# Performance work log

Hardware: AMD Instinct MI355X
Metric: run time of the kernel (lower is better)

## Reference

```python
import jax, jax.numpy as jnp
import numpy as np

B, LQ, LK, D = 8, 1024, 4096, 1024


def setup_inputs() -> dict:
    key = jax.random.key(0)
    k1, k2, k3, k4, k5, k6 = jax.random.split(key, 6)
    s = 1.0 / np.sqrt(D)
    return {
        "T": jax.random.normal(k1, (B, LQ, D), dtype=jnp.float32),
        "S": jax.random.normal(k2, (B, LK, D), dtype=jnp.float32),
        "Wq": jax.random.uniform(k3, (D, D), jnp.float32, -s, s),
        "Wk": jax.random.uniform(k4, (D, D), jnp.float32, -s, s),
        "Wv": jax.random.uniform(k5, (D, D), jnp.float32, -s, s),
        "Wo": jax.random.uniform(k6, (D, D), jnp.float32, -s, s),
    }


def reference(T, S, Wq, Wk, Wv, Wo):
    # Linear layers: y = x @ W.T (torch nn.Linear convention), bias=False
    q = jnp.einsum('bqd,ed->bqe', T, Wq)          # [B, LQ, D]
    k = jnp.einsum('bkd,ed->bke', S, Wk)          # [B, LK, D]
    v = jnp.einsum('bkd,ed->bke', S, Wv)          # [B, LK, D]
    scale = jnp.asarray(D, q.dtype) ** -0.5        # hidden_dim ** -0.5 (single head)
    attn = jnp.einsum('bqe,bke->bqk', q, k) * scale  # [B, LQ, LK]
    attn = jax.nn.softmax(attn, axis=-1)
    out = jnp.einsum('bqk,bke->bqe', attn, v)      # [B, LQ, D]
    return jnp.einsum('bqe,fe->bqf', out, Wo)      # output projection
```

## Files before the change

### kernel.cpp

```cpp
#include <hip/hip_runtime.h>
#include <stdint.h>

typedef __bf16 bf16;
typedef __bf16 bf16x8 __attribute__((ext_vector_type(8)));
typedef float f32x4 __attribute__((ext_vector_type(4)));

__device__ __forceinline__ void gload_lds16(const void* g, void* l) {
    __builtin_amdgcn_global_load_lds(
        (const __attribute__((address_space(1))) unsigned int*)g,
        (__attribute__((address_space(3))) unsigned int*)l, 16, 0, 0);
}

#define BAR()    asm volatile("s_barrier" ::: "memory")
#define WAITV(N) asm volatile("s_waitcnt vmcnt(" #N ")" ::: "memory")

#define STG(S, R, G, KOFF2, RS) do { \
    const bf16* _g = (G) + (KOFF2); \
    gload_lds16(_g,      &lds[S][R][d0]); \
    gload_lds16(_g + RS, &lds[S][R][d1]); \
  } while (0)

#define RD(S, R, OFF) (*(const bf16x8*)((const char*)&lds[S][R][0] + (OFF)))

#define MM(MB) \
    __builtin_amdgcn_s_setprio(1); \
    _Pragma("unroll") for (int mi = 0; mi < 4; ++mi) \
      _Pragma("unroll") for (int nj = 0; nj < 4; ++nj) \
        acc[MB + mi][nj] = __builtin_amdgcn_mfma_f32_16x16x32_bf16(av[mi], bv[nj], acc[MB + mi][nj], 0, 0, 0); \
    __builtin_amdgcn_s_setprio(0);

#define PH1(S, STGX) { \
    _Pragma("unroll") for (int nj = 0; nj < 4; ++nj) bv[nj] = RD(S, 2, bBase + nj * 1024); \
    _Pragma("unroll") for (int mi = 0; mi < 4; ++mi) av[mi] = RD(S, 0, aBase + mi * 1024); \
    STGX; BAR(); MM(0) BAR(); }

#define PH2(S, STGX) { \
    _Pragma("unroll") for (int mi = 0; mi < 4; ++mi) av[mi] = RD(S, 0, aBase + 4096 + mi * 1024); \
    STGX; BAR(); MM(4) BAR(); }

#define PH3(S, STGX) { \
    _Pragma("unroll") for (int nj = 0; nj < 4; ++nj) bv[nj] = RD(S, 3, bBase + nj * 1024); \
    _Pragma("unroll") for (int mi = 0; mi < 4; ++mi) av[mi] = RD(S, 1, aBase + mi * 1024); \
    STGX; BAR(); MM(0) BAR(); }

#define PH4(S, STGX, WT) { \
    _Pragma("unroll") for (int mi = 0; mi < 4; ++mi) av[mi] = RD(S, 1, aBase + 4096 + mi * 1024); \
    STGX; BAR(); MM(4) WT; BAR(); }

__global__ __launch_bounds__(512, 2)
void gemm_qkv(const bf16* __restrict__ Tb, const bf16* __restrict__ Sb,
              const bf16* __restrict__ Wq, const bf16* __restrict__ Wk,
              const bf16* __restrict__ Wv,
              bf16* __restrict__ Qo, bf16* __restrict__ Ko, bf16* __restrict__ VTo)
{
    __shared__ __align__(16) bf16 lds[2][4][8192];

    const int nwg  = gridDim.x;
    const int orig = blockIdx.x;
    const int q8   = nwg >> 3, r8 = nwg & 7;
    const int xcd  = orig & 7, lid = orig >> 3;
    const int p    = (xcd < r8 ? xcd * (q8 + 1) : r8 * (q8 + 1) + (xcd - r8) * q8) + lid;

    const bf16 *A, *Bw; bf16 *Co; bool vt = false;
    int lp;
    if (p < 512)       { lp = p;        A = Sb; Bw = Wk; Co = Ko; }
    else if (p < 1024) { lp = p - 512;  A = Sb; Bw = Wv; Co = VTo; vt = true; }
    else               { lp = p - 1024; A = Tb; Bw = Wq; Co = Qo; }

    const long rowb = (long)(lp >> 2) << 8;
    const long colb = (long)(lp & 3) << 8;

    const int t  = threadIdx.x;
    const int l  = t & 63;
    const int w  = t >> 6;
    const int wm = w >> 2;
    const int wn = w & 3;
    const int l15 = l & 15;
    const int r0  = (l >> 4) << 2;

    const int sL   = (t * 16) ^ (((t >> 3) & 3) << 4);
    const int srow = sL >> 6;
    const int sk   = (sL & 63) >> 1;
    const bf16* gA = A + (rowb + srow) * 1024 + sk;
    const bf16* gB = Bw + (colb + srow) * 1024 + sk;
    const long rA = 131072, rB = 131072;
    const int  d0 = t * 8, d1 = t * 8 + 4096;

    const int xl    = ((l >> 1) & 3) << 4;
    const int aBase = ((wm * 128 + l15) * 64 + ((l >> 4) << 4)) ^ xl;
    const int bBase = ((wn * 64  + l15) * 64 + ((l >> 4) << 4)) ^ xl;

    f32x4 acc[8][4] = {};
    bf16x8 av[4], bv[4];

    STG(0, 0, gA, 0,  rA);
    STG(0, 1, gA, 32, rA);
    STG(0, 2, gB, 0,  rB);
    STG(0, 3, gB, 32, rB);
    STG(1, 2, gB, 64, rB);
    STG(1, 0, gA, 64, rA);
    STG(1, 3, gB, 96, rB);
    WAITV(6);
    BAR();

    for (int i = 0; i < 7; ++i) {
        const int kb = i << 7;
        const int kn = kb + 128;
        PH1(0, STG(1, 1, gA, kb + 96, rA));
        PH2(0, STG(0, 2, gB, kn,      rB));
        PH3(0, STG(0, 0, gA, kn,      rA));
        PH4(0, STG(0, 3, gB, kn + 32, rB), WAITV(6));
        PH1(1, STG(0, 1, gA, kn + 32, rA));
        PH2(1, STG(1, 2, gB, kn + 64, rB));
        PH3(1, STG(1, 0, gA, kn + 64, rA));
        PH4(1, STG(1, 3, gB, kn + 96, rB), WAITV(6));
    }
    {
        PH1(0, STG(1, 1, gA, 7 * 128 + 96, rA));
        PH2(0, );
        PH3(0, );
        PH4(0, , WAITV(0));
        PH1(1, );
        PH2(1, );
        PH3(1, );
        PH4(1, , );
    }

    bf16* epi = &lds[0][0][0];
    const int rrow   = t >> 5;
    const int cchunk = (t & 31) << 3;
    const int myh = vt ? (wn >> 1) : wm;
#pragma unroll
    for (int h = 0; h < 2; ++h) {
        if (myh == h) {
#pragma unroll
            for (int mf = 0; mf < 8; ++mf)
#pragma unroll
              for (int nj = 0; nj < 4; ++nj)
#pragma unroll
                for (int r = 0; r < 4; ++r) {
                    int orow = wm * 128 + mf * 16 + r0 + r;
                    int ocol = wn * 64 + nj * 16 + l15;
                    if (vt) { int tmp = orow; orow = ocol; ocol = tmp; }
                    epi[(orow - h * 128) * 280 + ocol] = (bf16)acc[mf][nj][r];
                }
        }
        __syncthreads();
#pragma unroll
        for (int pp = 0; pp < 8; ++pp) {
            const int lrow = pp * 16 + rrow;
            const int row  = h * 128 + lrow;
            uint4 d = *(const uint4*)&epi[lrow * 280 + cchunk];
            if (!vt) {
                *(uint4*)&Co[(rowb + row) * 1024 + colb + cchunk] = d;
            } else {
                const long zz  = rowb >> 12;
                const long lk0 = (rowb & 4095) + cchunk;
                *(uint4*)&Co[zz * 4194304L + (colb + row) * 4096L + lk0] = d;
            }
        }
        __syncthreads();
    }
}

template<int OMODE>
__global__ __launch_bounds__(512, 2)
void gemm256(const bf16* __restrict__ A, const bf16* __restrict__ B,
             void* __restrict__ Cv, int K, int N,
             long batchA, long batchB, long batchC, float alpha,
             int nbx, int nby, int GC, int lda, int ldb,
             float* __restrict__ Smp)
{
    __shared__ __align__(16) bf16 lds[2][4][8192];

    const int nwg  = gridDim.x;
    const int orig = blockIdx.x;
    const int q8   = nwg >> 3, r8 = nwg & 7;
    const int xcd  = orig & 7, lid = orig >> 3;
    int p = (xcd < r8 ? xcd * (q8 + 1) : r8 * (q8 + 1) + (xcd - r8) * q8) + lid;

    int hv = 0;
    if constexpr (OMODE == 3) { hv = p >> 7; p &= 127; }
    const int kOff = hv << 11;

    const int perb = nbx * nby;
    const int z    = p / perb;
    const int pb   = p - z * perb;
    const int sw   = nby * GC;
    const int st   = pb / sw;
    const int rem  = pb - st * sw;
    const int by   = rem / GC;
    const int bx   = st * GC + (rem - by * GC);

    const long rowb = (long)by << 8;
    const long colb = (long)bx << 8;

    const int t  = threadIdx.x;
    const int l  = t & 63;
    const int w  = t >> 6;
    const int wm = w >> 2;
    const int wn = w & 3;
    const int l15 = l & 15;
    const int r0  = (l >> 4) << 2;

    const int sL   = (t * 16) ^ (((t >> 3) & 3) << 4);
    const int srow = sL >> 6;
    const int sk   = (sL & 63) >> 1;
    const bf16* gA = A + (long)z * batchA + (rowb + srow) * (long)lda + sk + kOff;
    const bf16* gB = B + (long)z * batchB + (colb + srow) * (long)ldb + sk + kOff;
    const long rA = 128L * lda;
    const long rB = 128L * ldb;
    const int  d0 = t * 8, d1 = t * 8 + 4096;

    const int xl    = ((l >> 1) & 3) << 4;
    const int aBase = ((wm * 128 + l15) * 64 + ((l >> 4) << 4)) ^ xl;
    const int bBase = ((wn * 64  + l15) * 64 + ((l >> 4) << 4)) ^ xl;

    f32x4 acc[8][4] = {};
    bf16x8 av[4], bv[4];

    STG(0, 0, gA, 0,  rA);
    STG(0, 1, gA, 32, rA);
    STG(0, 2, gB, 0,  rB);
    STG(0, 3, gB, 32, rB);
    STG(1, 2, gB, 64, rB);
    STG(1, 0, gA, 64, rA);
    STG(1, 3, gB, 96, rB);
    WAITV(6);
    BAR();

    const int NI = K >> 7;
    for (int i = 0; i < NI - 1; ++i) {
        const int kb = i << 7;
        const int kn = kb + 128;
        PH1(0, STG(1, 1, gA, kb + 96, rA));
        PH2(0, STG(0, 2, gB, kn,      rB));
        PH3(0, STG(0, 0, gA, kn,      rA));
        PH4(0, STG(0, 3, gB, kn + 32, rB), WAITV(6));
        PH1(1, STG(0, 1, gA, kn + 32, rA));
        PH2(1, STG(1, 2, gB, kn + 64, rB));
        PH3(1, STG(1, 0, gA, kn + 64, rA));
        PH4(1, STG(1, 3, gB, kn + 96, rB), WAITV(6));
    }
    {
        const int kb = (NI - 1) << 7;
        PH1(0, STG(1, 1, gA, kb + 96, rA));
        PH2(0, );
        PH3(0, );
        PH4(0, , WAITV(0));
        PH1(1, );
        PH2(1, );
        PH3(1, );
        PH4(1, , );
    }

    if constexpr (OMODE == 2) {
        const long cb0 = colb + wn * 64 + l15;
        const long rb0 = rowb + wm * 128 + r0;
#pragma unroll
        for (int mf = 0; mf < 8; ++mf)
#pragma unroll
          for (int nj = 0; nj < 4; ++nj) {
            const long col = cb0 + nj * 16;
#pragma unroll
            for (int r = 0; r < 4; ++r)
                ((float*)Cv)[(long)z * batchC + (rb0 + mf * 16 + r) * (long)N + col]
                    = acc[mf][nj][r] * alpha;
          }
    } else {
        bf16* Cb;
        if constexpr (OMODE == 3)
            Cb = (bf16*)Cv + (long)hv * 8388608 + (long)z * 1048576;
        else
            Cb = (bf16*)Cv + (long)z * batchC;
        bf16* epi = &lds[0][0][0];
        const int rrow   = t >> 5;
        const int cchunk = (t & 31) << 3;
#pragma unroll
        for (int h = 0; h < 2; ++h) {
            if (wm == h) {
#pragma unroll
                for (int mf = 0; mf < 8; ++mf)
#pragma unroll
                  for (int nj = 0; nj < 4; ++nj)
#pragma unroll
                    for (int r = 0; r < 4; ++r) {
                        float v = acc[mf][nj][r];
                        if constexpr (OMODE == 4) v = __expf(v * alpha);
                        const int orow = wm * 128 + mf * 16 + r0 + r;
                        const int ocol = wn * 64 + nj * 16 + l15;
                        epi[(orow - h * 128) * 280 + ocol] = (bf16)v;
                    }
            }
            __syncthreads();
#pragma unroll
            for (int pp = 0; pp < 8; ++pp) {
                const int lrow = pp * 16 + rrow;
                const int row  = h * 128 + lrow;
                union { uint4 u; bf16 h8[8]; } ud;
                ud.u = *(const uint4*)&epi[lrow * 280 + cchunk];
                *(uint4*)&Cb[(rowb + row) * (long)N + colb + cchunk] = ud.u;
                if constexpr (OMODE == 4) {
                    float s = 0.f;
#pragma unroll
                    for (int j = 0; j < 8; ++j) s += (float)ud.h8[j];
                    s += __shfl_xor(s, 1);
                    s += __shfl_xor(s, 2);
                    s += __shfl_xor(s, 4);
                    s += __shfl_xor(s, 8);
                    s += __shfl_xor(s, 16);
                    if ((t & 31) == 0)
                        Smp[((long)z * 1024 + rowb + row) * 16 + (colb >> 8)] = s;
                }
            }
            __syncthreads();
        }
    }
}

#undef STG
#undef RD
#undef MM
#undef PH1
#undef PH2
#undef PH3
#undef PH4

__global__ void cvt_all(const float* __restrict__ T, const float* __restrict__ S,
                        const float* __restrict__ Wq, const float* __restrict__ Wk,
                        const float* __restrict__ Wv, const float* __restrict__ Wo,
                        bf16* __restrict__ Tb, bf16* __restrict__ Sb,
                        bf16* __restrict__ Wb)
{
    const long i = (long)blockIdx.x * 256 + threadIdx.x;
    const float* src; bf16* dst; long j;
    if (i < 1048576)              { src = T; dst = Tb; j = i; }
    else if (i < 1048576+4194304) { src = S; dst = Sb; j = i - 1048576; }
    else {
        long k = i - 5242880;
        const int seg = (int)(k >> 17);
        j = k & 131071;
        src = seg == 0 ? Wq : seg == 1 ? Wk : seg == 2 ? Wv : Wo;
        dst = Wb + (long)seg * 1048576;
    }
    const float4* pp = (const float4*)src + j * 2;
    float4 a = pp[0], b = pp[1];
    union { bf16 h[8]; uint4 u; } o;
    o.h[0] = (bf16)a.x; o.h[1] = (bf16)a.y; o.h[2] = (bf16)a.z; o.h[3] = (bf16)a.w;
    o.h[4] = (bf16)b.x; o.h[5] = (bf16)b.y; o.h[6] = (bf16)b.z; o.h[7] = (bf16)b.w;
    ((uint4*)dst)[j] = o.u;
}

__global__ __launch_bounds__(256)
void sum16(const float* __restrict__ Smp, float* __restrict__ Sm)
{
    const int r = blockIdx.x * 256 + threadIdx.x;
    const float4* p4 = (const float4*)(Smp + (long)r * 16);
    float4 a = p4[0], b = p4[1], c = p4[2], d = p4[3];
    Sm[r] = ((a.x + a.y) + (a.z + a.w)) + ((b.x + b.y) + (b.z + b.w))
          + ((c.x + c.y) + (c.z + c.w)) + ((d.x + d.y) + (d.z + d.w));
}

__global__ void reduce_pv(const bf16* __restrict__ Pt, const float* __restrict__ sums,
                          bf16* __restrict__ Ob)
{
    const long i = (long)blockIdx.x * 256 + threadIdx.x;
    const float inv = 1.f / sums[i >> 7];
    union U { uint4 u; bf16 h[8]; };
    U a, b, o;
    a.u = ((const uint4*)Pt)[i];
    b.u = ((const uint4*)(Pt + 8388608))[i];
#pragma unroll
    for (int j = 0; j < 8; ++j)
        o.h[j] = (bf16)(((float)a.h[j] + (float)b.h[j]) * inv);
    ((uint4*)Ob)[i] = o.u;
}

extern "C" void kernel_launch(void* const* d_in, const int* in_sizes, int n_in,
                              void* d_out, int out_size, void* d_ws, size_t ws_size,
                              hipStream_t stream)
{
    (void)in_sizes; (void)n_in; (void)out_size; (void)ws_size;
    const float* T  = (const float*)d_in[0];
    const float* S  = (const float*)d_in[1];
    const float* Wq = (const float*)d_in[2];
    const float* Wk = (const float*)d_in[3];
    const float* Wv = (const float*)d_in[4];
    const float* Wo = (const float*)d_in[5];
    float* Y = (float*)d_out;
    char* ws = (char*)d_ws;

    bf16* Wqb = (bf16*)(ws + 0);
    bf16* Wkb = (bf16*)(ws + 2097152);
    bf16* Wvb = (bf16*)(ws + 4194304);
    bf16* Wob = (bf16*)(ws + 6291456);
    bf16* Tb  = (bf16*)(ws + 8388608);
    bf16* Ob  = Tb;
    bf16* Qb  = (bf16*)(ws + 25165824);
    bf16* Sb  = (bf16*)(ws + 41943040);
    bf16* Pb  = Sb;
    bf16* Kb  = (bf16*)(ws + 109051904);
    bf16* Pt  = Kb;
    bf16* VTb = (bf16*)(ws + 176160768);
    float* Sm  = (float*)ws;
    float* Smp = (float*)(ws + 2097152);

    cvt_all<<<22528, 256, 0, stream>>>(T, S, Wq, Wk, Wv, Wo, Tb, Sb, Wqb);

    gemm_qkv<<<1152, 512, 0, stream>>>(Tb, Sb, Wqb, Wkb, Wvb, Qb, Kb, VTb);

    gemm256<4><<<512, 512, 0, stream>>>(Qb, Kb, Pb, 1024, 4096,
        1024L * 1024, 4096L * 1024, 1024L * 4096, 0.03125f, 16, 4, 4, 1024, 1024, Smp);

    sum16<<<32, 256, 0, stream>>>(Smp, Sm);

    gemm256<3><<<256, 512, 0, stream>>>(Pb, VTb, Pt, 2048, 1024,
        1024L * 4096, 1024L * 4096, 1048576, 1.f, 4, 4, 4, 4096, 4096, nullptr);
    reduce_pv<<<4096, 256, 0, stream>>>(Pt, Sm, Ob);

    gemm256<2><<<128, 512, 0, stream>>>(Ob, Wob, Y, 1024, 1024,
        0, 0, 0, 1.f, 4, 32, 4, 1024, 1024, nullptr);
}
```

Baseline: 398.9 us.

## Fold split-K PV reduction and softmax normalization into output projection

```diff
diff --git a/kernel.cpp b/kernel.cpp
--- a/kernel.cpp
+++ b/kernel.cpp
@@ -260,17 +260,18 @@
 #pragma unroll
         for (int mf = 0; mf < 8; ++mf)
 #pragma unroll
-          for (int nj = 0; nj < 4; ++nj) {
-            const long col = cb0 + nj * 16;
-#pragma unroll
-            for (int r = 0; r < 4; ++r)
-                ((float*)Cv)[(long)z * batchC + (rb0 + mf * 16 + r) * (long)N + col]
-                    = acc[mf][nj][r] * alpha;
+          for (int r = 0; r < 4; ++r) {
+            const long row = rb0 + mf * 16 + r;
+            const float inv = 1.f / Smp[(long)z * 1024 + row];
+#pragma unroll
+            for (int nj = 0; nj < 4; ++nj)
+                ((float*)Cv)[(long)z * batchC + row * (long)N + cb0 + nj * 16]
+                    = acc[mf][nj][r] * inv;
           }
     } else {
         bf16* Cb;
         if constexpr (OMODE == 3)
-            Cb = (bf16*)Cv + (long)hv * 8388608 + (long)z * 1048576;
+            Cb = (bf16*)Cv + (long)z * batchC + (long)hv * 1024;
         else
             Cb = (bf16*)Cv + (long)z * batchC;
         bf16* epi = &lds[0][0][0];
@@ -351,6 +352,16 @@
     ((uint4*)dst)[j] = o.u;
 }
 
+__global__ void dup_wo(const bf16* __restrict__ Wo1, bf16* __restrict__ Wo2)
+{
+    const int i  = blockIdx.x * 256 + threadIdx.x;
+    const int f  = i >> 7;
+    const int e8 = (i & 127) << 3;
+    uint4 d = ((const uint4*)Wo1)[i];
+    *(uint4*)&Wo2[(long)f * 2048 + e8]        = d;
+    *(uint4*)&Wo2[(long)f * 2048 + 1024 + e8] = d;
+}
+
 __global__ __launch_bounds__(256)
 void sum16(const float* __restrict__ Smp, float* __restrict__ Sm)
 {
@@ -359,21 +370,6 @@
     float4 a = p4[0], b = p4[1], c = p4[2], d = p4[3];
     Sm[r] = ((a.x + a.y) + (a.z + a.w)) + ((b.x + b.y) + (b.z + b.w))
           + ((c.x + c.y) + (c.z + c.w)) + ((d.x + d.y) + (d.z + d.w));
-}
-
-__global__ void reduce_pv(const bf16* __restrict__ Pt, const float* __restrict__ sums,
-                          bf16* __restrict__ Ob)
-{
-    const long i = (long)blockIdx.x * 256 + threadIdx.x;
-    const float inv = 1.f / sums[i >> 7];
-    union U { uint4 u; bf16 h[8]; };
-    U a, b, o;
-    a.u = ((const uint4*)Pt)[i];
-    b.u = ((const uint4*)(Pt + 8388608))[i];
-#pragma unroll
-    for (int j = 0; j < 8; ++j)
-        o.h[j] = (bf16)(((float)a.h[j] + (float)b.h[j]) * inv);
-    ((uint4*)Ob)[i] = o.u;
 }
 
 extern "C" void kernel_launch(void* const* d_in, const int* in_sizes, int n_in,
@@ -395,8 +391,8 @@
     bf16* Wvb = (bf16*)(ws + 4194304);
     bf16* Wob = (bf16*)(ws + 6291456);
     bf16* Tb  = (bf16*)(ws + 8388608);
-    bf16* Ob  = Tb;
     bf16* Qb  = (bf16*)(ws + 25165824);
+    bf16* Wob2= Qb;
     bf16* Sb  = (bf16*)(ws + 41943040);
     bf16* Pb  = Sb;
     bf16* Kb  = (bf16*)(ws + 109051904);
@@ -412,12 +408,12 @@
     gemm256<4><<<512, 512, 0, stream>>>(Qb, Kb, Pb, 1024, 4096,
         1024L * 1024, 4096L * 1024, 1024L * 4096, 0.03125f, 16, 4, 4, 1024, 1024, Smp);
 
-    sum16<<<32, 256, 0, stream>>>(Smp, Sm);
-
-    gemm256<3><<<256, 512, 0, stream>>>(Pb, VTb, Pt, 2048, 1024,
-        1024L * 4096, 1024L * 4096, 1048576, 1.f, 4, 4, 4, 4096, 4096, nullptr);
-    reduce_pv<<<4096, 256, 0, stream>>>(Pt, Sm, Ob);
-
-    gemm256<2><<<128, 512, 0, stream>>>(Ob, Wob, Y, 1024, 1024,
-        0, 0, 0, 1.f, 4, 32, 4, 1024, 1024, nullptr);
-}
+    sum16 <<<32,  256, 0, stream>>>(Smp, Sm);
+    dup_wo<<<512, 256, 0, stream>>>(Wob, Wob2);
+
+    gemm256<3><<<256, 512, 0, stream>>>(Pb, VTb, Pt, 2048, 2048,
+        1024L * 4096, 1024L * 4096, 2097152, 1.f, 4, 4, 4, 4096, 4096, nullptr);
+
+    gemm256<2><<<128, 512, 0, stream>>>(Pt, Wob2, Y, 2048, 1024,
+        2097152, 0, 1048576, 1.f, 4, 4, 4, 2048, 2048, Sm);
+}
```

Result: slower. 417.8 us (+4.7%).
